# Performance work log

Measured on AMD Instinct MI355X. Metric: run time of the kernel, lower is better.

## Reference

```python
import jax, jax.numpy as jnp
import numpy as np

HIDDEN = 1024
HEADS = 16
D_K = HIDDEN // HEADS
B, S = 2, 2048


def setup_inputs() -> dict:
    key = jax.random.key(0)
    ks = jax.random.split(key, 11)
    sc = 1.0 / np.sqrt(HIDDEN)
    return {
        "query": jax.random.normal(ks[0], (B, S, HIDDEN), jnp.float32),
        "key": jax.random.normal(ks[1], (B, S, HIDDEN), jnp.float32),
        "value": jax.random.normal(ks[2], (B, S, HIDDEN), jnp.float32),
        "w_q": jax.random.normal(ks[3], (HIDDEN, HIDDEN), jnp.float32) * sc,
        "b_q": jax.random.normal(ks[4], (HIDDEN,), jnp.float32) * 0.02,
        "w_k": jax.random.normal(ks[5], (HIDDEN, HIDDEN), jnp.float32) * sc,
        "b_k": jax.random.normal(ks[6], (HIDDEN,), jnp.float32) * 0.02,
        "w_v": jax.random.normal(ks[7], (HIDDEN, HIDDEN), jnp.float32) * sc,
        "b_v": jax.random.normal(ks[8], (HIDDEN,), jnp.float32) * 0.02,
        "w_o": jax.random.normal(ks[9], (HIDDEN, HIDDEN), jnp.float32) * sc,
        "b_o": jax.random.normal(ks[10], (HIDDEN,), jnp.float32) * 0.02,
    }


def reference(query, key, value, w_q, b_q, w_k, b_k, w_v, b_v, w_o, b_o):
    b, s, _ = query.shape
    # linear projections (torch Linear: x @ W^T + b)
    q = query @ w_q.T + b_q
    k = key @ w_k.T + b_k
    v = value @ w_v.T + b_v
    # [B, H, S, D]
    q = q.reshape(b, s, HEADS, D_K).transpose(0, 2, 1, 3)
    k = k.reshape(b, s, HEADS, D_K).transpose(0, 2, 1, 3)
    v = v.reshape(b, s, HEADS, D_K).transpose(0, 2, 1, 3)
    scale = jnp.float32(1.0 / np.sqrt(D_K))
    scores = jnp.einsum('bhqd,bhkd->bhqk', q, k) * scale  # [B,H,S,S]
    probs = jax.nn.softmax(scores, axis=-1)
    y = jnp.einsum('bhqk,bhkd->bhqd', probs, v)
    y = y.transpose(0, 2, 1, 3).reshape(b, s, HIDDEN)
    return y @ w_o.T + b_o
```

## Files before the change

### kernel.cpp

```cpp
#include <hip/hip_runtime.h>
#include <hip/hip_bf16.h>
#include <math.h>

#define HIDDEN 1024
#define HEADS 16
#define DK 64
#define BB 2
#define SS 2048
#define MROWS (BB*SS)

typedef __attribute__((ext_vector_type(8))) short short8;
typedef __attribute__((ext_vector_type(4))) float f32x4;
typedef __attribute__((ext_vector_type(16))) float f32x16;
typedef __attribute__((ext_vector_type(4))) unsigned short ushort4_t;

static __device__ __forceinline__ unsigned short f2bf(float f) {
    unsigned int u = __float_as_uint(f);
    u += 0x7fffu + ((u >> 16) & 1u);
    return (unsigned short)(u >> 16);
}
static __device__ __forceinline__ float bf2f(unsigned short s) {
    return __uint_as_float(((unsigned int)s) << 16);
}

static __device__ __forceinline__ unsigned int cvtpk(float lo, float hi) {
    unsigned int r;
    asm volatile("v_cvt_pk_bf16_f32 %0, %1, %2" : "=v"(r) : "v"(lo), "v"(hi));
    return r;
}
static __device__ __forceinline__ void swap32(unsigned int& a, unsigned int& b) {
    asm volatile("v_permlane32_swap_b32 %0, %1" : "+v"(a), "+v"(b));
}
static __device__ __forceinline__ short8 pack_bf16x8(float4 lo, float4 hi) {
    union { unsigned int u[4]; short8 s; } r;
    r.u[0] = cvtpk(lo.x, lo.y);
    r.u[1] = cvtpk(lo.z, lo.w);
    r.u[2] = cvtpk(hi.x, hi.y);
    r.u[3] = cvtpk(hi.z, hi.w);
    return r.s;
}

__global__ __launch_bounds__(256, 3) void gemm_qkv(
    const float* __restrict__ Xq, const float* __restrict__ Xk, const float* __restrict__ Xv,
    const float* __restrict__ Wq, const float* __restrict__ Wk, const float* __restrict__ Wv,
    const float* __restrict__ bq, const float* __restrict__ bk, const float* __restrict__ bv,
    unsigned short* __restrict__ Qb, unsigned short* __restrict__ Kb, unsigned short* __restrict__ Vt,
    float scale_q) {
    __shared__ unsigned short As[128][40];
    __shared__ unsigned short Bs[128][40];
    const int lid = blockIdx.x + 8 * (blockIdx.y + 32 * blockIdx.z);
    const int c = lid & 7, i2 = lid >> 3;
    const int nb = i2 & 7;
    const int band = c * 12 + (i2 >> 3);
    const int yb = band & 31;
    const int z  = band >> 5;
    const float* A  = (z == 0) ? Xq : (z == 1) ? Xk : Xv;
    const float* Wt = (z == 0) ? Wq : (z == 1) ? Wk : Wv;
    const float* bias = (z == 0) ? bq : (z == 1) ? bk : bv;
    unsigned short* O = (z == 0) ? Qb : (z == 1) ? Kb : Vt;
    const float oscale = (z == 0) ? scale_q : 1.0f;

    const int t    = threadIdx.x;
    const int lane = t & 63;
    const int wave = t >> 6;
    const int m0 = yb * 128;
    const int n0 = nb * 128;
    const int row  = t >> 2;
    const int col8 = (t & 3) * 8;

    const int wm = (wave >> 1) * 64;
    const int wn = (wave & 1) * 64;
    const int lr = lane & 15;
    const int lk = (lane >> 4) * 8;

    f32x4 acc[4][4];
#pragma unroll
    for (int i = 0; i < 4; i++)
#pragma unroll
        for (int j = 0; j < 4; j++) acc[i][j] = f32x4{0.f, 0.f, 0.f, 0.f};

    for (int k0 = 0; k0 < HIDDEN; k0 += 32) {
        const float* a0 = A  + (size_t)(m0 + row)      * HIDDEN + k0 + col8;
        const float* a1 = A  + (size_t)(m0 + row + 64) * HIDDEN + k0 + col8;
        const float* w0 = Wt + (size_t)(n0 + row)      * HIDDEN + k0 + col8;
        const float* w1 = Wt + (size_t)(n0 + row + 64) * HIDDEN + k0 + col8;
        float4 a00 = reinterpret_cast<const float4*>(a0)[0];
        float4 a01 = reinterpret_cast<const float4*>(a0)[1];
        float4 a10 = reinterpret_cast<const float4*>(a1)[0];
        float4 a11 = reinterpret_cast<const float4*>(a1)[1];
        float4 w00 = reinterpret_cast<const float4*>(w0)[0];
        float4 w01 = reinterpret_cast<const float4*>(w0)[1];
        float4 w10 = reinterpret_cast<const float4*>(w1)[0];
        float4 w11 = reinterpret_cast<const float4*>(w1)[1];
        __syncthreads();
        *reinterpret_cast<short8*>(&As[row][col8])      = pack_bf16x8(a00, a01);
        *reinterpret_cast<short8*>(&As[row + 64][col8]) = pack_bf16x8(a10, a11);
        *reinterpret_cast<short8*>(&Bs[row][col8])      = pack_bf16x8(w00, w01);
        *reinterpret_cast<short8*>(&Bs[row + 64][col8]) = pack_bf16x8(w10, w11);
        __syncthreads();
        short8 af[4], bfr[4];
#pragma unroll
        for (int i = 0; i < 4; i++) af[i]  = *reinterpret_cast<const short8*>(&As[wm + i * 16 + lr][lk]);
#pragma unroll
        for (int j = 0; j < 4; j++) bfr[j] = *reinterpret_cast<const short8*>(&Bs[wn + j * 16 + lr][lk]);
#pragma unroll
        for (int i = 0; i < 4; i++)
#pragma unroll
            for (int j = 0; j < 4; j++)
                acc[i][j] = __builtin_amdgcn_mfma_f32_16x16x32_bf16(af[i], bfr[j], acc[i][j], 0, 0, 0);
    }

#pragma unroll
    for (int i = 0; i < 4; i++) {
        int mrow = m0 + wm + i * 16 + (lane >> 4) * 4;
#pragma unroll
        for (int j = 0; j < 4; j++) {
            int ncol = n0 + wn + j * 16 + lr;
            float bvv = bias[ncol];
            int b_ = mrow >> 11;
            int h_ = ncol >> 6;
            int d_ = ncol & 63;
            if (z != 2) {
#pragma unroll
                for (int r = 0; r < 4; r++) {
                    int s_ = (mrow + r) & 2047;
                    O[(((size_t)(b_ * HEADS + h_)) * SS + s_) * DK + d_] = f2bf((acc[i][j][r] + bvv) * oscale);
                }
            } else {
                int s0 = mrow & 2047;
                ushort4_t pk;
                pk.x = f2bf(acc[i][j][0] + bvv);
                pk.y = f2bf(acc[i][j][1] + bvv);
                pk.z = f2bf(acc[i][j][2] + bvv);
                pk.w = f2bf(acc[i][j][3] + bvv);
                *reinterpret_cast<ushort4_t*>(O + (((size_t)(b_ * HEADS + h_) * DK + d_) * SS + s0)) = pk;
            }
        }
    }
}

__global__ __launch_bounds__(256) void gemm_o(const unsigned short* __restrict__ A,
                                              const float* __restrict__ Wt,
                                              const float* __restrict__ bias,
                                              float* __restrict__ O) {
    __shared__ unsigned short As[128][40];
    __shared__ unsigned short Bs[64][40];
    const int lid = blockIdx.x + 16 * blockIdx.y;
    const int c = lid & 7, i2 = lid >> 3;
    const int nb = i2 & 15;
    const int band = c * 4 + (i2 >> 4);
    const int t    = threadIdx.x;
    const int lane = t & 63;
    const int wave = t >> 6;
    const int m0 = band * 128;
    const int n0 = nb * 64;
    const int row  = t >> 2;
    const int col8 = (t & 3) * 8;

    const int wm = wave * 32;
    const int lr = lane & 15;
    const int lk = (lane >> 4) * 8;

    f32x4 acc[2][4];
#pragma unroll
    for (int i = 0; i < 2; i++)
#pragma unroll
        for (int j = 0; j < 4; j++) acc[i][j] = f32x4{0.f, 0.f, 0.f, 0.f};

    for (int k0 = 0; k0 < HIDDEN; k0 += 32) {
        short8 av0 = *reinterpret_cast<const short8*>(A + (size_t)(m0 + row)      * HIDDEN + k0 + col8);
        short8 av1 = *reinterpret_cast<const short8*>(A + (size_t)(m0 + row + 64) * HIDDEN + k0 + col8);
        const float* w0 = Wt + (size_t)(n0 + row) * HIDDEN + k0 + col8;
        float4 w00 = reinterpret_cast<const float4*>(w0)[0];
        float4 w01 = reinterpret_cast<const float4*>(w0)[1];
        __syncthreads();
        *reinterpret_cast<short8*>(&As[row][col8])      = av0;
        *reinterpret_cast<short8*>(&As[row + 64][col8]) = av1;
        *reinterpret_cast<short8*>(&Bs[row][col8])      = pack_bf16x8(w00, w01);
        __syncthreads();
        short8 af[2], bfr[4];
#pragma unroll
        for (int i = 0; i < 2; i++) af[i]  = *reinterpret_cast<const short8*>(&As[wm + i * 16 + lr][lk]);
#pragma unroll
        for (int j = 0; j < 4; j++) bfr[j] = *reinterpret_cast<const short8*>(&Bs[j * 16 + lr][lk]);
#pragma unroll
        for (int i = 0; i < 2; i++)
#pragma unroll
            for (int j = 0; j < 4; j++)
                acc[i][j] = __builtin_amdgcn_mfma_f32_16x16x32_bf16(af[i], bfr[j], acc[i][j], 0, 0, 0);
    }

#pragma unroll
    for (int i = 0; i < 2; i++) {
        int mrow = m0 + wm + i * 16 + (lane >> 4) * 4;
#pragma unroll
        for (int j = 0; j < 4; j++) {
            int ncol = n0 + j * 16 + lr;
            float bvv = bias[ncol];
#pragma unroll
            for (int r = 0; r < 4; r++)
                O[(size_t)(mrow + r) * HIDDEN + ncol] = acc[i][j][r] + bvv;
        }
    }
}

__global__ __launch_bounds__(256, 4) void attn_kernel(const unsigned short* __restrict__ Qb,
                                                      const unsigned short* __restrict__ Kb,
                                                      const unsigned short* __restrict__ Vt,
                                                      unsigned short* __restrict__ Yb0,
                                                      unsigned short* __restrict__ Yb1,
                                                      float2* __restrict__ ml) {
    __shared__ __attribute__((aligned(16))) unsigned short Ksh[2][64 * 64];
    __shared__ __attribute__((aligned(16))) unsigned short Vsh[2][64 * 64];
    __shared__ float Lsh[4][32];

    const int t    = threadIdx.x;
    const int lane = t & 63;
    const int wave = t >> 6;
    const int fid  = blockIdx.x;
    const int c    = fid & 7;
    const int i    = fid >> 3;
    const int qblk = i & 15;
    const int pair = c * 8 + (i >> 4);
    const int bh   = pair >> 1;
    const int kvh  = pair & 1;
    const int b_ = bh >> 4, h_ = bh & 15;
    const int qbase = qblk * 128 + wave * 32;
    const int kvbase = kvh << 10;
    const unsigned short* Qp = Qb + (size_t)bh * SS * DK;
    const unsigned short* Kp = Kb + (size_t)bh * SS * DK;
    const unsigned short* Vp = Vt + (size_t)bh * DK * SS;
    const int lq = lane & 31;
    const int hi = lane >> 5;
    const int sr = lane >> 3;
    const int cs = (lane & 7) ^ sr;

    short8 qf[4];
#pragma unroll
    for (int cc = 0; cc < 4; cc++)
        qf[cc] = *reinterpret_cast<const short8*>(Qp + (size_t)(qbase + lq) * DK + cc * 16 + hi * 8);

    f32x16 acc0, acc1;
#pragma unroll
    for (int r = 0; r < 16; r++) { acc0[r] = 0.f; acc1[r] = 0.f; }
    float mi = -INFINITY, li = 0.f;

#define STAGE(BUF, KV0) do {                                                                 \
    __builtin_amdgcn_global_load_lds(                                                        \
        (const __attribute__((address_space(1))) unsigned int*)(Kp + (size_t)((KV0) + wave * 16 + sr) * DK + cs * 8), \
        (__attribute__((address_space(3))) unsigned int*)&Ksh[BUF][(wave * 16) * 64], 16, 0, 0); \
    __builtin_amdgcn_global_load_lds(                                                        \
        (const __attribute__((address_space(1))) unsigned int*)(Kp + (size_t)((KV0) + wave * 16 + 8 + sr) * DK + cs * 8), \
        (__attribute__((address_space(3))) unsigned int*)&Ksh[BUF][(wave * 16 + 8) * 64], 16, 0, 0); \
    __builtin_amdgcn_global_load_lds(                                                        \
        (const __attribute__((address_space(1))) unsigned int*)(Vp + (size_t)(wave * 16 + sr) * SS + (KV0) + cs * 8), \
        (__attribute__((address_space(3))) unsigned int*)&Vsh[BUF][(wave * 16) * 64], 16, 0, 0); \
    __builtin_amdgcn_global_load_lds(                                                        \
        (const __attribute__((address_space(1))) unsigned int*)(Vp + (size_t)(wave * 16 + 8 + sr) * SS + (KV0) + cs * 8), \
        (__attribute__((address_space(3))) unsigned int*)&Vsh[BUF][(wave * 16 + 8) * 64], 16, 0, 0); \
} while (0)

    STAGE(0, kvbase);
    __syncthreads();

    for (int kv0 = kvbase; kv0 < kvbase + 1024; kv0 += 64) {
        const int cur = (kv0 >> 6) & 1;
        if (kv0 + 64 < kvbase + 1024) STAGE(cur ^ 1, kv0 + 64);

        f32x16 sv0, sv1;
#pragma unroll
        for (int r = 0; r < 16; r++) { sv0[r] = 0.f; sv1[r] = 0.f; }
#pragma unroll
        for (int cc = 0; cc < 4; cc++) {
            short8 kf0 = *reinterpret_cast<const short8*>(
                &Ksh[cur][lq * 64 + (((2 * cc + hi) ^ (lq & 7)) << 3)]);
            short8 kf1 = *reinterpret_cast<const short8*>(
                &Ksh[cur][(32 + lq) * 64 + (((2 * cc + hi) ^ (lq & 7)) << 3)]);
            sv0 = __builtin_amdgcn_mfma_f32_32x32x16_bf16(kf0, qf[cc], sv0, 0, 0, 0);
            sv1 = __builtin_amdgcn_mfma_f32_32x32x16_bf16(kf1, qf[cc], sv1, 0, 0, 0);
        }

        float vmax = sv0[0];
#pragma unroll
        for (int r = 0; r < 16; r++) { vmax = fmaxf(vmax, sv0[r]); vmax = fmaxf(vmax, sv1[r]); }
        vmax = fmaxf(vmax, __shfl_xor(vmax, 32));
        if (!__all(vmax <= mi + 8.0f)) {
            float mnew = fmaxf(mi, vmax);
            float sc = __builtin_amdgcn_exp2f(mi - mnew);
            li *= sc;
            acc0 = acc0 * sc;
            acc1 = acc1 * sc;
            mi = mnew;
        }
        float pt[2][16];
        float rs = 0.f;
#pragma unroll
        for (int r = 0; r < 16; r++) {
            pt[0][r] = __builtin_amdgcn_exp2f(sv0[r] - mi);
            pt[1][r] = __builtin_amdgcn_exp2f(sv1[r] - mi);
            rs += pt[0][r] + pt[1][r];
        }
        rs += __shfl_xor(rs, 32);
        li += rs;

        short8 fragP[4];
#pragma unroll
        for (int tt = 0; tt < 2; tt++)
#pragma unroll
            for (int cl = 0; cl < 2; cl++) {
                unsigned int w0 = cvtpk(pt[tt][cl * 8 + 0], pt[tt][cl * 8 + 1]);
                unsigned int w1 = cvtpk(pt[tt][cl * 8 + 2], pt[tt][cl * 8 + 3]);
                unsigned int w2 = cvtpk(pt[tt][cl * 8 + 4], pt[tt][cl * 8 + 5]);
                unsigned int w3 = cvtpk(pt[tt][cl * 8 + 6], pt[tt][cl * 8 + 7]);
                swap32(w0, w2);
                swap32(w1, w3);
                union { unsigned int u[4]; short8 s; } f;
                f.u[0] = w0; f.u[1] = w1; f.u[2] = w2; f.u[3] = w3;
                fragP[tt * 2 + cl] = f.s;
            }

#pragma unroll
        for (int cc = 0; cc < 4; cc++) {
            short8 vf0 = *reinterpret_cast<const short8*>(
                &Vsh[cur][lq * 64 + (((2 * cc + hi) ^ (lq & 7)) << 3)]);
            short8 vf1 = *reinterpret_cast<const short8*>(
                &Vsh[cur][(32 + lq) * 64 + (((2 * cc + hi) ^ (lq & 7)) << 3)]);
            acc0 = __builtin_amdgcn_mfma_f32_32x32x16_bf16(fragP[cc], vf0, acc0, 0, 0, 0);
            acc1 = __builtin_amdgcn_mfma_f32_32x32x16_bf16(fragP[cc], vf1, acc1, 0, 0, 0);
        }
        __syncthreads();
    }
#undef STAGE

    unsigned short* Yp = kvh ? Yb1 : Yb0;
    if (lane < 32) {
        Lsh[wave][lq] = 1.0f / li;
        ml[(((size_t)kvh * 32 + bh) << 11) + qbase + lq] = float2{mi, li};
    }
    __syncthreads();
#pragma unroll
    for (int r = 0; r < 16; r++) {
        int qr = (r & 3) + 8 * (r >> 2) + 4 * hi;
        float inv = Lsh[wave][qr];
        size_t base = ((size_t)b_ * SS + qbase + qr) * HIDDEN + h_ * 64 + lq;
        Yp[base]      = f2bf(acc0[r] * inv);
        Yp[base + 32] = f2bf(acc1[r] * inv);
    }
}

__global__ __launch_bounds__(256) void combine_halves(const unsigned short* __restrict__ Yb0,
                                                      const unsigned short* __restrict__ Yb1,
                                                      const float2* __restrict__ ml,
                                                      unsigned short* __restrict__ Yb) {
    int j = blockIdx.x * 256 + threadIdx.x;
    int chunk = j & 127;
    int s = (j >> 7) & 2047;
    int b = j >> 18;
    int h = chunk >> 3;
    int bh = b * 16 + h;
    float2 m0 = ml[((size_t)bh << 11) + s];
    float2 m1 = ml[(((size_t)32 + bh) << 11) + s];
    float M = fmaxf(m0.x, m1.x);
    float l0 = m0.y * __builtin_amdgcn_exp2f(m0.x - M);
    float l1 = m1.y * __builtin_amdgcn_exp2f(m1.x - M);
    float inv = 1.0f / (l0 + l1);
    float w0 = l0 * inv, w1 = l1 * inv;
    short8 a = reinterpret_cast<const short8*>(Yb0)[j];
    short8 bb = reinterpret_cast<const short8*>(Yb1)[j];
    union { unsigned int u[4]; short8 s8; } o;
#pragma unroll
    for (int k = 0; k < 4; k++) {
        float lo = w0 * bf2f((unsigned short)a[2 * k])     + w1 * bf2f((unsigned short)bb[2 * k]);
        float hi = w0 * bf2f((unsigned short)a[2 * k + 1]) + w1 * bf2f((unsigned short)bb[2 * k + 1]);
        o.u[k] = cvtpk(lo, hi);
    }
    reinterpret_cast<short8*>(Yb)[j] = o.s8;
}

extern "C" void kernel_launch(void* const* d_in, const int* in_sizes, int n_in,
                              void* d_out, int out_size, void* d_ws, size_t ws_size,
                              hipStream_t stream) {
    const float* query = (const float*)d_in[0];
    const float* key_  = (const float*)d_in[1];
    const float* value = (const float*)d_in[2];
    const float* w_q = (const float*)d_in[3];
    const float* b_q = (const float*)d_in[4];
    const float* w_k = (const float*)d_in[5];
    const float* b_k = (const float*)d_in[6];
    const float* w_v = (const float*)d_in[7];
    const float* b_v = (const float*)d_in[8];
    const float* w_o = (const float*)d_in[9];
    const float* b_o = (const float*)d_in[10];

    const size_t SZ_X = (size_t)MROWS * HIDDEN * 2;
    char* ws = (char*)d_ws;
    unsigned short* Qb  = (unsigned short*)(ws);
    unsigned short* Kbf = (unsigned short*)(ws + SZ_X);
    unsigned short* Vt  = (unsigned short*)(ws + 2 * SZ_X);
    unsigned short* Yb0 = (unsigned short*)(ws + 3 * SZ_X);
    unsigned short* Yb1 = (unsigned short*)(ws + 4 * SZ_X);
    unsigned short* Yb  = (unsigned short*)(ws + 5 * SZ_X);
    float2*         ml  = (float2*)(ws + 6 * SZ_X);

    const float SCALE_Q = 0.125f * 1.4426950408889634f;
    gemm_qkv<<<dim3(8, 32, 3), 256, 0, stream>>>(
        query, key_, value, w_q, w_k, w_v, b_q, b_k, b_v, Qb, Kbf, Vt, SCALE_Q);

    attn_kernel<<<dim3(1024), 256, 0, stream>>>(Qb, Kbf, Vt, Yb0, Yb1, ml);

    combine_halves<<<dim3(2048), 256, 0, stream>>>(Yb0, Yb1, ml, Yb);

    gemm_o<<<dim3(16, 32), 256, 0, stream>>>(Yb, w_o, b_o, (float*)d_out);
}
```

Measured before the change: 129.1 us.

## Pre-cast QKV inputs to bf16 and stage GEMM tiles via direct global-to-LDS loads

Adds a separate cast kernel that converts the three activation tensors and three weight matrices to bf16 in workspace. The QKV GEMM then reads bf16 and loads tiles straight into LDS with global_load_lds, using an XOR-swizzled layout and K-step 64. This removes the per-tile float-to-bf16 conversion and register staging, and halves the bytes the GEMM reads from global memory on each tile pass. The cost is an extra launch that reads all fp32 inputs once and writes bf16 copies (about 30 MB of traffic), plus more workspace. The main loop still waits on a barrier after each load, with no double buffering.

```diff
diff --git a/kernel.cpp b/kernel.cpp
--- a/kernel.cpp
+++ b/kernel.cpp
@@ -40,22 +40,45 @@
     return r.s;
 }
 
-__global__ __launch_bounds__(256, 3) void gemm_qkv(
-    const float* __restrict__ Xq, const float* __restrict__ Xk, const float* __restrict__ Xv,
-    const float* __restrict__ Wq, const float* __restrict__ Wk, const float* __restrict__ Wv,
+__global__ __launch_bounds__(256) void cast_all(
+    const float* __restrict__ q, const float* __restrict__ k, const float* __restrict__ v,
+    const float* __restrict__ wq, const float* __restrict__ wk, const float* __restrict__ wv,
+    unsigned short* __restrict__ Xq, unsigned short* __restrict__ Xk, unsigned short* __restrict__ Xv,
+    unsigned short* __restrict__ Wq, unsigned short* __restrict__ Wk, unsigned short* __restrict__ Wv) {
+    int i = blockIdx.x * 256 + threadIdx.x;
+    const float* src; unsigned short* dst; int off;
+    if (i < (3 << 20)) {
+        int w = i >> 20; off = i & ((1 << 20) - 1);
+        src = (w == 0) ? q : (w == 1) ? k : v;
+        dst = (w == 0) ? Xq : (w == 1) ? Xk : Xv;
+    } else {
+        int j = i - (3 << 20);
+        int w = j >> 18; off = j & ((1 << 18) - 1);
+        src = (w == 0) ? wq : (w == 1) ? wk : wv;
+        dst = (w == 0) ? Wq : (w == 1) ? Wk : Wv;
+    }
+    float4 f = reinterpret_cast<const float4*>(src)[off];
+    ushort4_t o;
+    o.x = f2bf(f.x); o.y = f2bf(f.y); o.z = f2bf(f.z); o.w = f2bf(f.w);
+    reinterpret_cast<ushort4_t*>(dst)[off] = o;
+}
+
+__global__ __launch_bounds__(256, 4) void gemm_qkv(
+    const unsigned short* __restrict__ Xq, const unsigned short* __restrict__ Xk, const unsigned short* __restrict__ Xv,
+    const unsigned short* __restrict__ Wq, const unsigned short* __restrict__ Wk, const unsigned short* __restrict__ Wv,
     const float* __restrict__ bq, const float* __restrict__ bk, const float* __restrict__ bv,
     unsigned short* __restrict__ Qb, unsigned short* __restrict__ Kb, unsigned short* __restrict__ Vt,
     float scale_q) {
-    __shared__ unsigned short As[128][40];
-    __shared__ unsigned short Bs[128][40];
+    __shared__ __attribute__((aligned(16))) unsigned short As[128 * 64];
+    __shared__ __attribute__((aligned(16))) unsigned short Bs[128 * 64];
     const int lid = blockIdx.x + 8 * (blockIdx.y + 32 * blockIdx.z);
     const int c = lid & 7, i2 = lid >> 3;
     const int nb = i2 & 7;
     const int band = c * 12 + (i2 >> 3);
     const int yb = band & 31;
     const int z  = band >> 5;
-    const float* A  = (z == 0) ? Xq : (z == 1) ? Xk : Xv;
-    const float* Wt = (z == 0) ? Wq : (z == 1) ? Wk : Wv;
+    const unsigned short* A  = (z == 0) ? Xq : (z == 1) ? Xk : Xv;
+    const unsigned short* Wt = (z == 0) ? Wq : (z == 1) ? Wk : Wv;
     const float* bias = (z == 0) ? bq : (z == 1) ? bk : bv;
     unsigned short* O = (z == 0) ? Qb : (z == 1) ? Kb : Vt;
     const float oscale = (z == 0) ? scale_q : 1.0f;
@@ -65,13 +88,13 @@
     const int wave = t >> 6;
     const int m0 = yb * 128;
     const int n0 = nb * 128;
-    const int row  = t >> 2;
-    const int col8 = (t & 3) * 8;
 
     const int wm = (wave >> 1) * 64;
     const int wn = (wave & 1) * 64;
     const int lr = lane & 15;
-    const int lk = (lane >> 4) * 8;
+    const int g  = lane >> 4;
+    const int sr = lane >> 3;
+    const int cs = (lane & 7) ^ sr;
 
     f32x4 acc[4][4];
 #pragma unroll
@@ -79,36 +102,42 @@
 #pragma unroll
         for (int j = 0; j < 4; j++) acc[i][j] = f32x4{0.f, 0.f, 0.f, 0.f};
 
-    for (int k0 = 0; k0 < HIDDEN; k0 += 32) {
-        const float* a0 = A  + (size_t)(m0 + row)      * HIDDEN + k0 + col8;
-        const float* a1 = A  + (size_t)(m0 + row + 64) * HIDDEN + k0 + col8;
-        const float* w0 = Wt + (size_t)(n0 + row)      * HIDDEN + k0 + col8;
-        const float* w1 = Wt + (size_t)(n0 + row + 64) * HIDDEN + k0 + col8;
-        float4 a00 = reinterpret_cast<const float4*>(a0)[0];
-        float4 a01 = reinterpret_cast<const float4*>(a0)[1];
-        float4 a10 = reinterpret_cast<const float4*>(a1)[0];
-        float4 a11 = reinterpret_cast<const float4*>(a1)[1];
-        float4 w00 = reinterpret_cast<const float4*>(w0)[0];
-        float4 w01 = reinterpret_cast<const float4*>(w0)[1];
-        float4 w10 = reinterpret_cast<const float4*>(w1)[0];
-        float4 w11 = reinterpret_cast<const float4*>(w1)[1];
+#define GSTAGE(K0) do {                                                                      \
+    _Pragma("unroll")                                                                        \
+    for (int jj = 0; jj < 4; jj++) {                                                         \
+        int rb = wave * 32 + jj * 8;                                                         \
+        __builtin_amdgcn_global_load_lds(                                                    \
+            (const __attribute__((address_space(1))) unsigned int*)(A + (size_t)(m0 + rb + sr) * HIDDEN + (K0) + cs * 8), \
+            (__attribute__((address_space(3))) unsigned int*)&As[rb * 64], 16, 0, 0);        \
+        __builtin_amdgcn_global_load_lds(                                                    \
+            (const __attribute__((address_space(1))) unsigned int*)(Wt + (size_t)(n0 + rb + sr) * HIDDEN + (K0) + cs * 8), \
+            (__attribute__((address_space(3))) unsigned int*)&Bs[rb * 64], 16, 0, 0);        \
+    }                                                                                        \
+} while (0)
+
+    for (int k0 = 0; k0 < HIDDEN; k0 += 64) {
+        GSTAGE(k0);
         __syncthreads();
-        *reinterpret_cast<short8*>(&As[row][col8])      = pack_bf16x8(a00, a01);
-        *reinterpret_cast<short8*>(&As[row + 64][col8]) = pack_bf16x8(a10, a11);
-        *reinterpret_cast<short8*>(&Bs[row][col8])      = pack_bf16x8(w00, w01);
-        *reinterpret_cast<short8*>(&Bs[row + 64][col8]) = pack_bf16x8(w10, w11);
+#pragma unroll
+        for (int kk = 0; kk < 2; kk++) {
+            short8 af[4], bfr[4];
+#pragma unroll
+            for (int i = 0; i < 4; i++)
+                af[i] = *reinterpret_cast<const short8*>(
+                    &As[(wm + i * 16 + lr) * 64 + (((kk * 4 + g) ^ (lr & 7)) << 3)]);
+#pragma unroll
+            for (int j = 0; j < 4; j++)
+                bfr[j] = *reinterpret_cast<const short8*>(
+                    &Bs[(wn + j * 16 + lr) * 64 + (((kk * 4 + g) ^ (lr & 7)) << 3)]);
+#pragma unroll
+            for (int i = 0; i < 4; i++)
+#pragma unroll
+                for (int j = 0; j < 4; j++)
+                    acc[i][j] = __builtin_amdgcn_mfma_f32_16x16x32_bf16(af[i], bfr[j], acc[i][j], 0, 0, 0);
+        }
         __syncthreads();
-        short8 af[4], bfr[4];
-#pragma unroll
-        for (int i = 0; i < 4; i++) af[i]  = *reinterpret_cast<const short8*>(&As[wm + i * 16 + lr][lk]);
-#pragma unroll
-        for (int j = 0; j < 4; j++) bfr[j] = *reinterpret_cast<const short8*>(&Bs[wn + j * 16 + lr][lk]);
-#pragma unroll
-        for (int i = 0; i < 4; i++)
-#pragma unroll
-            for (int j = 0; j < 4; j++)
-                acc[i][j] = __builtin_amdgcn_mfma_f32_16x16x32_bf16(af[i], bfr[j], acc[i][j], 0, 0, 0);
-    }
+    }
+#undef GSTAGE
 
 #pragma unroll
     for (int i = 0; i < 4; i++) {
@@ -393,18 +422,28 @@
     const float* b_o = (const float*)d_in[10];
 
     const size_t SZ_X = (size_t)MROWS * HIDDEN * 2;
+    const size_t SZ_W = (size_t)HIDDEN * HIDDEN * 2;
     char* ws = (char*)d_ws;
-    unsigned short* Qb  = (unsigned short*)(ws);
-    unsigned short* Kbf = (unsigned short*)(ws + SZ_X);
-    unsigned short* Vt  = (unsigned short*)(ws + 2 * SZ_X);
-    unsigned short* Yb0 = (unsigned short*)(ws + 3 * SZ_X);
-    unsigned short* Yb1 = (unsigned short*)(ws + 4 * SZ_X);
-    unsigned short* Yb  = (unsigned short*)(ws + 5 * SZ_X);
-    float2*         ml  = (float2*)(ws + 6 * SZ_X);
+    unsigned short* Xq = (unsigned short*)(ws);
+    unsigned short* Xk = (unsigned short*)(ws + SZ_X);
+    unsigned short* Xv = (unsigned short*)(ws + 2 * SZ_X);
+    unsigned short* Wq = (unsigned short*)(ws + 3 * SZ_X);
+    unsigned short* Wk = (unsigned short*)(ws + 3 * SZ_X + SZ_W);
+    unsigned short* Wv = (unsigned short*)(ws + 3 * SZ_X + 2 * SZ_W);
+    unsigned short* Qb  = (unsigned short*)(ws + 3 * SZ_X + 3 * SZ_W);
+    unsigned short* Kbf = (unsigned short*)(ws + 4 * SZ_X + 3 * SZ_W);
+    unsigned short* Vt  = (unsigned short*)(ws + 5 * SZ_X + 3 * SZ_W);
+    unsigned short* Yb0 = (unsigned short*)(ws + 6 * SZ_X + 3 * SZ_W);
+    unsigned short* Yb1 = (unsigned short*)(ws + 7 * SZ_X + 3 * SZ_W);
+    unsigned short* Yb  = (unsigned short*)(ws + 8 * SZ_X + 3 * SZ_W);
+    float2*         ml  = (float2*)(ws + 9 * SZ_X + 3 * SZ_W);
+
+    cast_all<<<15360, 256, 0, stream>>>(query, key_, value, w_q, w_k, w_v,
+                                        Xq, Xk, Xv, Wq, Wk, Wv);
 
     const float SCALE_Q = 0.125f * 1.4426950408889634f;
     gemm_qkv<<<dim3(8, 32, 3), 256, 0, stream>>>(
-        query, key_, value, w_q, w_k, w_v, b_q, b_k, b_v, Qb, Kbf, Vt, SCALE_Q);
+        Xq, Xk, Xv, Wq, Wk, Wv, b_q, b_k, b_v, Qb, Kbf, Vt, SCALE_Q);
 
     attn_kernel<<<dim3(1024), 256, 0, stream>>>(Qb, Kbf, Vt, Yb0, Yb1, ml);
 
```

Result: no change. 131.1 us (+1.5%).
